# Kernel tuning notes

Measured on AMD Instinct MI355X. Metric: run time of the kernel, lower is better.

## Reference

```python
import jax, jax.numpy as jnp
import numpy as np

N, E, G = 50000, 800000, 500
D, H, L, C, P = 256, 128, 2, 2, 128


def gcn(h, W, b, src, dst, ew, n):
    # PyG GCNConv: x@W, add self-loops (weight 1), sym-normalized aggregation at dst, + bias
    x = h @ W
    deg = jnp.ones((n,), x.dtype).at[dst].add(ew)  # self-loop contributes 1
    dinv = jax.lax.rsqrt(deg)
    norm = dinv[src] * ew * dinv[dst]
    out = jax.ops.segment_sum(x[src] * norm[:, None], dst, num_segments=n)
    out = out + x * (dinv * dinv)[:, None]  # self-loop message
    return out + b


def setup_inputs() -> dict:
    key = jax.random.key(0)
    ks = iter(jax.random.split(key, 64))

    def p(shape, s=0.05):
        return jax.random.normal(next(ks), shape, jnp.float32) * s

    inp = {
        'x': jax.random.normal(next(ks), (N, D), jnp.float32),
        'edge_index': jax.random.randint(next(ks), (2, E), 0, N),
        'edge_weight': jax.random.uniform(next(ks), (E,), jnp.float32),
        'batch': jnp.sort(jax.random.randint(next(ks), (N,), 0, G)),
        'eeg_mask': jax.random.randint(next(ks), (N,), 0, 2).astype(jnp.int32),
        'num_graphs': G,
        'eeg_W': p((D, H)), 'eeg_b': jnp.zeros((H,), jnp.float32),
        'fnirs_W': p((D, H)), 'fnirs_b': jnp.zeros((H,), jnp.float32),
        'edge_W1': p((H + 1, 64)), 'edge_b1': jnp.zeros((64,), jnp.float32),
        'edge_W2': p((64, 1)), 'edge_b2': jnp.zeros((1,), jnp.float32),
        'conv_intra_W': p((L, H, H)), 'conv_intra_b': jnp.zeros((L, H), jnp.float32),
        'conv_cross_W': p((L, H, H)), 'conv_cross_b': jnp.zeros((L, H), jnp.float32),
        'rel_gate': jnp.zeros((L,), jnp.float32),
        'bn_gamma': jnp.ones((L, H), jnp.float32), 'bn_beta': jnp.zeros((L, H), jnp.float32),
        'co_W1': p((3 * H, H)), 'co_b1': jnp.zeros((H,), jnp.float32),
        'co_W2': p((H, 2)), 'co_b2': jnp.zeros((2,), jnp.float32),
        'gate_W1': p((2 * H, H)), 'gate_b1': jnp.zeros((H,), jnp.float32),
        'gate_W2': p((H, 1)), 'gate_b2': jnp.zeros((1,), jnp.float32),
        'cls_W1': p((H, H // 2)), 'cls_b1': jnp.zeros((H // 2,), jnp.float32),
        'cls_W2': p((H // 2, C)), 'cls_b2': jnp.zeros((C,), jnp.float32),
        'pe_W1': p((H, H)), 'pe_b1': jnp.zeros((H,), jnp.float32),
        'pe_W2': p((H, P)), 'pe_b2': jnp.zeros((P,), jnp.float32),
        'pf_W1': p((H, H)), 'pf_b1': jnp.zeros((H,), jnp.float32),
        'pf_W2': p((H, P)), 'pf_b2': jnp.zeros((P,), jnp.float32),
    }
    return inp


def reference(x, edge_index, edge_weight, batch, eeg_mask, num_graphs,
              eeg_W, eeg_b, fnirs_W, fnirs_b,
              edge_W1, edge_b1, edge_W2, edge_b2,
              conv_intra_W, conv_intra_b, conv_cross_W, conv_cross_b,
              rel_gate, bn_gamma, bn_beta,
              co_W1, co_b1, co_W2, co_b2,
              gate_W1, gate_b1, gate_W2, gate_b2,
              cls_W1, cls_b1, cls_W2, cls_b2,
              pe_W1, pe_b1, pe_W2, pe_b2,
              pf_W1, pf_b1, pf_W2, pf_b2):
    n = x.shape[0]
    src, dst = edge_index[0], edge_index[1]
    em = eeg_mask.astype(bool)
    emf = em.astype(x.dtype)
    # modality-aware projection (select per node)
    h = jnp.where(em[:, None], jax.nn.relu(x @ eeg_W + eeg_b), jax.nn.relu(x @ fnirs_W + fnirs_b))
    # edge modulation: MLP on (|h_src - h_dst|, w)
    diff = jnp.abs(h[src] - h[dst])  # [E, H]
    eh = jax.nn.relu(jnp.concatenate([diff, edge_weight[:, None]], axis=1) @ edge_W1 + edge_b1)
    g = jax.nn.sigmoid((eh @ edge_W2 + edge_b2)[:, 0])
    ew_hat = edge_weight * jnp.clip(g, 0.2, 1.2)
    # intra/cross relation split via weight masking (same math as edge subsetting)
    intra = (em[src] == em[dst]).astype(x.dtype)
    ew_intra = ew_hat * intra
    ew_cross = ew_hat * (1.0 - intra)
    for l in range(conv_intra_W.shape[0]):
        hi = gcn(h, conv_intra_W[l], conv_intra_b[l], src, dst, ew_intra, n)
        hc = gcn(h, conv_cross_W[l], conv_cross_b[l], src, dst, ew_cross, n)
        h = hi + jax.nn.sigmoid(rel_gate[l]) * hc
        mu = h.mean(0)
        var = h.var(0)  # biased, as in torch BN training
        h = bn_gamma[l] * (h - mu) * jax.lax.rsqrt(var + 1e-5) + bn_beta[l]
        h = jax.nn.relu(h)  # dropout: eval mode (identity)

    def pool(w):
        s = jax.ops.segment_sum(h * w[:, None], batch, num_segments=num_graphs)
        c = jax.ops.segment_sum(w, batch, num_segments=num_graphs)
        return s / jnp.maximum(c, 1.0)[:, None]

    h_global = pool(jnp.ones((n,), x.dtype))
    h_e = pool(emf)
    h_f = pool(1.0 - emf)
    co = jnp.concatenate([h_e, h_f, h_e * h_f], axis=-1)
    alpha = jax.nn.sigmoid(jax.nn.relu(co @ co_W1 + co_b1) @ co_W2 + co_b2)
    alpha = alpha / (alpha.sum(-1, keepdims=True) + 1e-6)
    h_cr = alpha[:, :1] * h_e + alpha[:, 1:] * h_f
    gte = jax.nn.sigmoid(jax.nn.relu(jnp.concatenate([h_cr, h_global], -1) @ gate_W1 + gate_b1) @ gate_W2 + gate_b2)
    h_final = gte * h_cr + (1.0 - gte) * h_global
    logits = jax.nn.relu(h_final @ cls_W1 + cls_b1) @ cls_W2 + cls_b2

    def l2n(z):
        return z / jnp.maximum(jnp.linalg.norm(z, axis=-1, keepdims=True), 1e-12)

    z_e = l2n(jax.nn.relu(h_e @ pe_W1 + pe_b1) @ pe_W2 + pe_b2)
    z_f = l2n(jax.nn.relu(h_f @ pf_W1 + pf_b1) @ pf_W2 + pf_b2)
    return logits, z_e, z_f
```

## Files before the change

### kernel.cpp

```cpp
#include <hip/hip_runtime.h>
#include <math.h>

#define H 128
#define D 256

typedef __attribute__((ext_vector_type(8))) short bf16x8;
typedef __attribute__((ext_vector_type(4))) float f32x4;

__device__ __forceinline__ float sigmoidf_(float x){ return 1.0f/(1.0f+__expf(-x)); }

__device__ __forceinline__ unsigned int bfr_(float f){
  unsigned int u = __float_as_uint(f);
  return (u + 0x7fffu + ((u>>16)&1u)) >> 16;
}

__device__ __forceinline__ void split2(float a, float b, unsigned &hi, unsigned &lo){
  unsigned ha = bfr_(a), hb2 = bfr_(b);
  float fa = __uint_as_float(ha<<16), fb = __uint_as_float(hb2<<16);
  unsigned la = bfr_(a - fa), lb = bfr_(b - fb);
  hi = ha | (hb2<<16); lo = la | (lb<<16);
}

__device__ __forceinline__ unsigned pair_dft(unsigned a, unsigned b){
  float a0 = __uint_as_float(a<<16), a1 = __uint_as_float(a & 0xffff0000u);
  float b0 = __uint_as_float(b<<16), b1 = __uint_as_float(b & 0xffff0000u);
  unsigned d0 = __float_as_uint(fabsf(a0-b0));
  unsigned d1 = __float_as_uint(fabsf(a1-b1));
  return __builtin_amdgcn_perm(d1, d0, 0x07060302);
}

__global__ void k_prepall(const float* __restrict__ eegW, const float* __restrict__ fnW,
                          const float* __restrict__ cIW, const float* __restrict__ cCW,
                          const float* __restrict__ eW1,
                          unsigned short* WeF, unsigned short* WfF,
                          unsigned short* WIf0, unsigned short* WCf0,
                          unsigned short* WIf1, unsigned short* WCf1,
                          unsigned short* W1b)
{
  int b = blockIdx.x;
  int t = threadIdx.x;
  if (b < 64){
    const float* W; unsigned short* out; int ksteps; int boff;
    if (b < 16){ W=eegW; out=WeF; ksteps=8; boff=b; }
    else if (b < 32){ W=fnW; out=WfF; ksteps=8; boff=b-16; }
    else if (b < 40){ W=cIW;        out=WIf0; ksteps=4; boff=b-32; }
    else if (b < 48){ W=cCW;        out=WCf0; ksteps=4; boff=b-40; }
    else if (b < 56){ W=cIW+16384;  out=WIf1; ksteps=4; boff=b-48; }
    else            { W=cCW+16384;  out=WCf1; ksteps=4; boff=b-56; }
    int id = boff*256 + t;
    if (id >= ksteps*8*64) return;
    int lane = id & 63;
    int mfrag = (id>>6) & 7;
    int kstep = id >> 9;
    int col = mfrag*16 + (lane&15);
    int k0 = kstep*32 + (lane>>4)*8;
    unsigned short* oh = out + (size_t)(((kstep*8+mfrag)*2+0)*64 + lane)*8;
    unsigned short* ol = out + (size_t)(((kstep*8+mfrag)*2+1)*64 + lane)*8;
    #pragma unroll
    for (int j=0;j<8;j++){
      float w = W[(size_t)(k0+j)*128 + col];
      unsigned h16 = bfr_(w);
      float hf = __uint_as_float(h16<<16);
      oh[j] = (unsigned short)h16;
      ol[j] = (unsigned short)bfr_(w - hf);
    }
  } else {
    for (int it=0; it<4; it++){
      int le = it*256 + t;
      int f = le >> 6, lane = le & 63;
      int kstep = f >> 2, n = f & 3;
      int col = n*16 + (lane & 15);
      int k0 = kstep*32 + ((lane>>4)&3)*8;
      unsigned short* op = W1b + (size_t)le*8;
      #pragma unroll
      for (int j=0;j<8;j++)
        op[j] = (unsigned short)bfr_(eW1[(size_t)(k0+j)*64 + col]);
    }
  }
}

__global__ __launch_bounds__(256) void k_projm(
    const float* __restrict__ x, const int* __restrict__ em,
    const unsigned short* __restrict__ WeF, const float* __restrict__ be,
    const unsigned short* __restrict__ WfF, const float* __restrict__ bf,
    float* __restrict__ h, unsigned int* __restrict__ hb, int N)
{
  int t = threadIdx.x;
  int lane = t & 63;
  int base = (blockIdx.x*4 + (t>>6))*16;
  if (base >= N) return;
  int node = base + (lane & 15);
  int nodeL = min(node, N-1);
  int ko = lane >> 4;

  f32x4 accE[8], accF[8];
  #pragma unroll
  for (int mf=0;mf<8;mf++){ accE[mf]=(f32x4){0.f,0.f,0.f,0.f}; accF[mf]=(f32x4){0.f,0.f,0.f,0.f}; }

  const bf16x8* we = reinterpret_cast<const bf16x8*>(WeF);
  const bf16x8* wf = reinterpret_cast<const bf16x8*>(WfF);
  const float4* xr0 = reinterpret_cast<const float4*>(x + (size_t)nodeL*D + ko*8);

  float4 nv0 = xr0[0], nv1 = xr0[1];
  #pragma unroll
  for (int kstep=0;kstep<8;kstep++){
    float4 v0 = nv0, v1 = nv1;
    if (kstep < 7){
      nv0 = xr0[(kstep+1)*8];
      nv1 = xr0[(kstep+1)*8 + 1];
    }
    uint4 hiu, lou;
    split2(v0.x, v0.y, hiu.x, lou.x);
    split2(v0.z, v0.w, hiu.y, lou.y);
    split2(v1.x, v1.y, hiu.z, lou.z);
    split2(v1.z, v1.w, hiu.w, lou.w);
    bf16x8 Bhi = *reinterpret_cast<bf16x8*>(&hiu);
    bf16x8 Blo = *reinterpret_cast<bf16x8*>(&lou);
    #pragma unroll
    for (int mf=0;mf<8;mf++){
      int fb = (kstep*8+mf)*2;
      bf16x8 aEh = we[(size_t)fb*64 + lane];
      bf16x8 aEl = we[(size_t)(fb+1)*64 + lane];
      accE[mf] = __builtin_amdgcn_mfma_f32_16x16x32_bf16(aEh, Bhi, accE[mf], 0,0,0);
      accE[mf] = __builtin_amdgcn_mfma_f32_16x16x32_bf16(aEh, Blo, accE[mf], 0,0,0);
      accE[mf] = __builtin_amdgcn_mfma_f32_16x16x32_bf16(aEl, Bhi, accE[mf], 0,0,0);
      bf16x8 aFh = wf[(size_t)fb*64 + lane];
      bf16x8 aFl = wf[(size_t)(fb+1)*64 + lane];
      accF[mf] = __builtin_amdgcn_mfma_f32_16x16x32_bf16(aFh, Bhi, accF[mf], 0,0,0);
      accF[mf] = __builtin_amdgcn_mfma_f32_16x16x32_bf16(aFh, Blo, accF[mf], 0,0,0);
      accF[mf] = __builtin_amdgcn_mfma_f32_16x16x32_bf16(aFl, Bhi, accF[mf], 0,0,0);
    }
  }
  if (node >= N) return;
  bool e = em[node] != 0;
  #pragma unroll
  for (int mf=0;mf<8;mf++){
    float sv[4];
    #pragma unroll
    for (int r=0;r<4;r++){
      int ch = mf*16 + ko*4 + r;
      float vE = accE[mf][r] + be[ch];
      float vF = accF[mf][r] + bf[ch];
      sv[r] = fmaxf(e ? vE : vF, 0.f);
    }
    float2* hp = reinterpret_cast<float2*>(h + (size_t)node*H + mf*16 + ko*4);
    hp[0] = make_float2(sv[0], sv[1]);
    hp[1] = make_float2(sv[2], sv[3]);
    unsigned int* hbp = hb + (size_t)node*64 + mf*8 + ko*2;
    hbp[0] = bfr_(sv[0]) | (bfr_(sv[1])<<16);
    hbp[1] = bfr_(sv[2]) | (bfr_(sv[3])<<16);
  }
}

__global__ __launch_bounds__(256) void k_gemm2m(
    const float* __restrict__ A,
    const unsigned short* __restrict__ WIf, const unsigned short* __restrict__ WCf,
    const float* __restrict__ bna, const float* __restrict__ bnb2,
    unsigned int* __restrict__ tIb, unsigned int* __restrict__ tCb, int N)
{
  int t = threadIdx.x;
  int lane = t & 63;
  int base = (blockIdx.x*4 + (t>>6))*16;
  if (base >= N) return;
  int node = base + (lane & 15);
  int nodeL = min(node, N-1);
  int ko = lane >> 4;

  f32x4 accI[8], accC[8];
  #pragma unroll
  for (int mf=0;mf<8;mf++){ accI[mf]=(f32x4){0.f,0.f,0.f,0.f}; accC[mf]=(f32x4){0.f,0.f,0.f,0.f}; }

  const bf16x8* wi = reinterpret_cast<const bf16x8*>(WIf);
  const bf16x8* wc = reinterpret_cast<const bf16x8*>(WCf);
  bool doBN = (bna != nullptr);

  #pragma unroll
  for (int kstep=0;kstep<4;kstep++){
    const float4* ar = reinterpret_cast<const float4*>(A + (size_t)nodeL*H + kstep*32 + ko*8);
    float4 v0 = ar[0], v1 = ar[1];
    if (doBN){
      int ch = kstep*32 + ko*8;
      const float4* a4 = reinterpret_cast<const float4*>(bna + ch);
      const float4* b4 = reinterpret_cast<const float4*>(bnb2 + ch);
      float4 a0 = a4[0], a1 = a4[1], bb0 = b4[0], bb1 = b4[1];
      v0.x = fmaxf(fmaf(a0.x, v0.x, bb0.x), 0.f);
      v0.y = fmaxf(fmaf(a0.y, v0.y, bb0.y), 0.f);
      v0.z = fmaxf(fmaf(a0.z, v0.z, bb0.z), 0.f);
      v0.w = fmaxf(fmaf(a0.w, v0.w, bb0.w), 0.f);
      v1.x = fmaxf(fmaf(a1.x, v1.x, bb1.x), 0.f);
      v1.y = fmaxf(fmaf(a1.y, v1.y, bb1.y), 0.f);
      v1.z = fmaxf(fmaf(a1.z, v1.z, bb1.z), 0.f);
      v1.w = fmaxf(fmaf(a1.w, v1.w, bb1.w), 0.f);
    }
    uint4 hiu, lou;
    split2(v0.x, v0.y, hiu.x, lou.x);
    split2(v0.z, v0.w, hiu.y, lou.y);
    split2(v1.x, v1.y, hiu.z, lou.z);
    split2(v1.z, v1.w, hiu.w, lou.w);
    bf16x8 Bhi = *reinterpret_cast<bf16x8*>(&hiu);
    bf16x8 Blo = *reinterpret_cast<bf16x8*>(&lou);
    #pragma unroll
    for (int mf=0;mf<8;mf++){
      int fb = (kstep*8+mf)*2;
      bf16x8 aIh = wi[(size_t)fb*64 + lane];
      bf16x8 aIl = wi[(size_t)(fb+1)*64 + lane];
      accI[mf] = __builtin_amdgcn_mfma_f32_16x16x32_bf16(aIh, Bhi, accI[mf], 0,0,0);
      accI[mf] = __builtin_amdgcn_mfma_f32_16x16x32_bf16(aIh, Blo, accI[mf], 0,0,0);
      accI[mf] = __builtin_amdgcn_mfma_f32_16x16x32_bf16(aIl, Bhi, accI[mf], 0,0,0);
      bf16x8 aCh = wc[(size_t)fb*64 + lane];
      bf16x8 aCl = wc[(size_t)(fb+1)*64 + lane];
      accC[mf] = __builtin_amdgcn_mfma_f32_16x16x32_bf16(aCh, Bhi, accC[mf], 0,0,0);
      accC[mf] = __builtin_amdgcn_mfma_f32_16x16x32_bf16(aCh, Blo, accC[mf], 0,0,0);
      accC[mf] = __builtin_amdgcn_mfma_f32_16x16x32_bf16(aCl, Bhi, accC[mf], 0,0,0);
    }
  }
  if (node >= N) return;
  #pragma unroll
  for (int mf=0;mf<8;mf++){
    unsigned int* ti = tIb + (size_t)node*64 + mf*8 + ko*2;
    unsigned int* tc = tCb + (size_t)node*64 + mf*8 + ko*2;
    ti[0] = bfr_(accI[mf][0]) | (bfr_(accI[mf][1])<<16);
    ti[1] = bfr_(accI[mf][2]) | (bfr_(accI[mf][3])<<16);
    tc[0] = bfr_(accC[mf][0]) | (bfr_(accC[mf][1])<<16);
    tc[1] = bfr_(accC[mf][2]) | (bfr_(accC[mf][3])<<16);
  }
}

__global__ void k_hist(const int* __restrict__ ei, int* __restrict__ cnt, int E){
  int e = blockIdx.x*blockDim.x + threadIdx.x;
  if (e < E) atomicAdd(cnt + ei[E+e], 1);
}

__global__ __launch_bounds__(1024) void k_scanA(const int* __restrict__ cnt,
                                                int* __restrict__ start,
                                                int* __restrict__ bsum, int N){
  __shared__ int wsum[16];
  int t = threadIdx.x;
  int lane = t & 63, wid = t >> 6;
  int i = blockIdx.x*1024 + t;
  int v = (i < N) ? cnt[i] : 0;
  int s = v;
  #pragma unroll
  for (int d=1; d<64; d<<=1){
    int u = __shfl_up(s, d, 64);
    if (lane >= d) s += u;
  }
  if (lane == 63) wsum[wid] = s;
  __syncthreads();
  if (wid == 0){
    int w = (lane < 16) ? wsum[lane] : 0;
    #pragma unroll
    for (int d=1; d<16; d<<=1){
      int u = __shfl_up(w, d, 64);
      if (lane >= d) w += u;
    }
    if (lane < 16) wsum[lane] = w;
  }
  __syncthreads();
  int incl = s + ((wid > 0) ? wsum[wid-1] : 0);
  if (i < N) start[i] = incl - v;
  if (t == 1023) bsum[blockIdx.x] = incl;
}

__global__ __launch_bounds__(1024) void k_scanC(int* __restrict__ start,
                                                const int* __restrict__ bsum,
                                                int N, int nb){
  int b = blockIdx.x, t = threadIdx.x;
  int o = 0;
  for (int j=0;j<b;j++) o += bsum[j];
  int i = b*1024 + t;
  if (i < N) start[i] += o;
  if (b == nb-1 && t == 0) start[N] = o + bsum[b];
}

__global__ void k_fill2(const int* __restrict__ ei, const int* __restrict__ em,
                        const float* __restrict__ ew,
                        const int* __restrict__ start, int* __restrict__ wcnt,
                        int* __restrict__ csr_sc, int* __restrict__ csr_d,
                        float* __restrict__ csr_w, int E){
  int e = blockIdx.x*blockDim.x + threadIdx.x;
  if (e >= E) return;
  int s = ei[e], d = ei[E+e];
  int chan = (em[s] == em[d]) ? 0 : 1;
  int pos = start[d] + atomicAdd(wcnt + d, 1);
  csr_sc[pos] = (s<<1) | chan;
  csr_d[pos] = d;
  csr_w[pos] = ew[e];
}

__global__ __launch_bounds__(256) void k_edgem(
    const unsigned int* __restrict__ hb,
    const int* __restrict__ csr_sc, const int* __restrict__ csr_d,
    const float* __restrict__ csr_w, const unsigned short* __restrict__ W1b,
    const float* __restrict__ W1, const float* __restrict__ b1,
    const float* __restrict__ W2, const float* __restrict__ b2,
    float* __restrict__ csr_cf,
    float* __restrict__ degI, float* __restrict__ degC, int E)
{
  __shared__ uint4 wlds[1024];
  int t = threadIdx.x;
  {
    const uint4* src = reinterpret_cast<const uint4*>(W1b);
    #pragma unroll
    for (int i=0;i<4;i++) wlds[i*256 + t] = src[i*256 + t];
  }
  __syncthreads();

  int lane = t & 63;
  int base0 = (blockIdx.x*4 + (t>>6)) * 32;
  if (base0 >= E) return;

  int colbase = lane & 15;
  int ko = lane >> 4;
  float w1l[4], b1v[4], w2v[4];
  #pragma unroll
  for (int n=0;n<4;n++){
    int col = n*16 + colbase;
    w1l[n] = W1[(size_t)128*64 + col];
    b1v[n] = b1[col];
    w2v[n] = W2[col];
  }
  float bb2 = b2[0];

  uint4 us[2][4], ud[2][4];
  #pragma unroll
  for (int eg=0; eg<2; eg++){
    int e = min(base0 + eg*16 + colbase, E-1);
    int s = csr_sc[e] >> 1;
    int d = csr_d[e];
    const uint4* hsp = reinterpret_cast<const uint4*>(hb + (size_t)s*64);
    const uint4* hdp = reinterpret_cast<const uint4*>(hb + (size_t)d*64);
    #pragma unroll
    for (int kstep=0;kstep<4;kstep++){
      us[eg][kstep] = hsp[kstep*4 + ko];
      ud[eg][kstep] = hdp[kstep*4 + ko];
    }
  }

  const bf16x8* wl = reinterpret_cast<const bf16x8*>(wlds);
  #pragma unroll
  for (int eg=0; eg<2; eg++){
    int base = base0 + eg*16;
    if (base >= E) break;

    f32x4 acc[4];
    #pragma unroll
    for (int n=0;n<4;n++) acc[n] = (f32x4){0.f,0.f,0.f,0.f};

    #pragma unroll
    for (int kstep=0;kstep<4;kstep++){
      uint4 pa;
      pa.x = pair_dft(us[eg][kstep].x, ud[eg][kstep].x);
      pa.y = pair_dft(us[eg][kstep].y, ud[eg][kstep].y);
      pa.z = pair_dft(us[eg][kstep].z, ud[eg][kstep].z);
      pa.w = pair_dft(us[eg][kstep].w, ud[eg][kstep].w);
      bf16x8 a = *reinterpret_cast<bf16x8*>(&pa);
      #pragma unroll
      for (int n=0;n<4;n++)
        acc[n] = __builtin_amdgcn_mfma_f32_16x16x32_bf16(a, wl[(kstep*4+n)*64 + lane], acc[n], 0,0,0);
    }

    float wgtr[4];
    #pragma unroll
    for (int r=0;r<4;r++)
      wgtr[r] = csr_w[min(base + ko*4 + r, E-1)];

    float part[4] = {0.f,0.f,0.f,0.f};
    #pragma unroll
    for (int n=0;n<4;n++){
      #pragma unroll
      for (int r=0;r<4;r++){
        float v = fmaxf(acc[n][r] + fmaf(wgtr[r], w1l[n], b1v[n]), 0.f);
        part[r] = fmaf(v, w2v[n], part[r]);
      }
    }
    #pragma unroll
    for (int m=1;m<16;m<<=1){
      #pragma unroll
      for (int r=0;r<4;r++) part[r] += __shfl_xor(part[r], m, 64);
    }

    if (colbase == 0){
      #pragma unroll
      for (int r=0;r<4;r++){
        int ee = base + ko*4 + r;
        if (ee < E){
          float g = sigmoidf_(part[r] + bb2);
          g = fminf(fmaxf(g, 0.2f), 1.2f);
          float ehat = wgtr[r] * g;
          csr_cf[ee] = ehat;
          int sc2 = csr_sc[ee];
          atomicAdd(((sc2&1) ? degC : degI) + csr_d[ee], ehat);
        }
      }
    }
  }
}

__global__ void k_dinv(const float* __restrict__ degI, const float* __restrict__ degC,
                       float* dinvI, float* dinvC, int N){
  int i = blockIdx.x*blockDim.x + threadIdx.x;
  if (i < N){
    dinvI[i] = rsqrtf(1.f + degI[i]);
    dinvC[i] = rsqrtf(1.f + degC[i]);
  }
}

__global__ void k_scale(const int* __restrict__ csr_sc, const int* __restrict__ csr_d,
                        const float* __restrict__ dinvI, const float* __restrict__ dinvC,
                        float* __restrict__ csr_cf, int E){
  int k = blockIdx.x*blockDim.x + threadIdx.x;
  if (k >= E) return;
  int sc = csr_sc[k];
  int s = sc>>1;
  int d = csr_d[k];
  const float* dv = (sc&1) ? dinvC : dinvI;
  csr_cf[k] *= dv[s]*dv[d];
}

__global__ void k_bnab(const float* __restrict__ bnsum, const float* __restrict__ bnsq,
                       const float* __restrict__ gamma, const float* __restrict__ beta,
                       float invN, float* __restrict__ bna, float* __restrict__ bnb2){
  int j = threadIdx.x;
  float mu = bnsum[j]*invN;
  float var = bnsq[j]*invN - mu*mu;
  float r = rsqrtf(var + 1e-5f);
  float a = gamma[j]*r;
  bna[j] = a;
  bnb2[j] = beta[j] - a*mu;
}

__global__ __launch_bounds__(256) void k_aggrb(
    const unsigned int* __restrict__ tIb, const unsigned int* __restrict__ tCb,
    const int* __restrict__ start, const int* __restrict__ csr_sc,
    const float* __restrict__ csr_cf,
    const float* __restrict__ dinvI, const float* __restrict__ dinvC,
    const float* __restrict__ bI, const float* __restrict__ bC,
    const float* __restrict__ relg, int l,
    float* __restrict__ h, int N)
{
  int lane = threadIdx.x & 63;
  int d = blockIdx.x*4 + (threadIdx.x>>6);
  if (d >= N) return;
  float sig = sigmoidf_(relg[l]);
  int k0 = start[d], k1 = start[d+1];
  float ax=0.f, ay=0.f;
  int k = k0;
  for (; k+8 <= k1; k += 8){
    unsigned vv[8]; float cc[8];
    #pragma unroll
    for (int u=0;u<8;u++){
      int sc = csr_sc[k+u];
      float cf = csr_cf[k+u];
      vv[u] = ((sc&1) ? tCb : tIb)[(size_t)(sc>>1)*64 + lane];
      cc[u] = (sc&1) ? sig*cf : cf;
    }
    #pragma unroll
    for (int u=0;u<8;u++){
      ax = fmaf(cc[u], __uint_as_float(vv[u]<<16), ax);
      ay = fmaf(cc[u], __uint_as_float(vv[u] & 0xffff0000u), ay);
    }
  }
  for (; k < k1; ++k){
    int sc = csr_sc[k];
    float cf = csr_cf[k];
    unsigned v = ((sc&1) ? tCb : tIb)[(size_t)(sc>>1)*64 + lane];
    float ce = (sc&1) ? sig*cf : cf;
    ax = fmaf(ce, __uint_as_float(v<<16), ax);
    ay = fmaf(ce, __uint_as_float(v & 0xffff0000u), ay);
  }
  float diI = dinvI[d], diC = dinvC[d];
  float rI = diI*diI, rC = diC*diC;
  unsigned vi = tIb[(size_t)d*64 + lane];
  unsigned vc = tCb[(size_t)d*64 + lane];
  int off = lane*2;
  float ox = fmaf(__uint_as_float(vi<<16), rI, bI[off])
           + sig*fmaf(__uint_as_float(vc<<16), rC, bC[off]) + ax;
  float oy = fmaf(__uint_as_float(vi & 0xffff0000u), rI, bI[off+1])
           + sig*fmaf(__uint_as_float(vc & 0xffff0000u), rC, bC[off+1]) + ay;
  *reinterpret_cast<float2*>(h + (size_t)d*H + off) = make_float2(ox, oy);
}

__global__ __launch_bounds__(128) void k_stats(const float* __restrict__ h,
    float* __restrict__ bnsum, float* __restrict__ bnsq, int N, int nper)
{
  int j = threadIdx.x;
  int n0 = blockIdx.x*nper, n1 = min(n0+nper, N);
  if (n0 >= N) return;
  float sl=0.f, sq=0.f;
  for (int n=n0;n<n1;n++){
    float v = h[(size_t)n*H+j];
    sl += v; sq = fmaf(v,v,sq);
  }
  atomicAdd(bnsum+j, sl); atomicAdd(bnsq+j, sq);
}

__global__ __launch_bounds__(128) void k_poolbn(
    const float* __restrict__ h, const int* __restrict__ batch, const int* __restrict__ em,
    const float* __restrict__ bnsum, const float* __restrict__ bnsq,
    const float* __restrict__ gamma, const float* __restrict__ beta, float invN,
    float* __restrict__ sumE, float* __restrict__ sumF,
    float* __restrict__ cntE, float* __restrict__ cntF, int N, int nper)
{
  int j = threadIdx.x;
  int n0 = blockIdx.x*nper, n1 = min(n0+nper, N);
  if (n0 >= N) return;
  float mu = bnsum[j]*invN;
  float var = bnsq[j]*invN - mu*mu;
  float rr = rsqrtf(var + 1e-5f);
  float ga = gamma[j], be = beta[j];
  float aE=0.f, aF=0.f, ce=0.f, cfc=0.f;
  int cg = batch[n0];
  for (int n=n0;n<n1;n++){
    int g = batch[n];
    if (g != cg){
      atomicAdd(sumE+(size_t)cg*H+j, aE);
      atomicAdd(sumF+(size_t)cg*H+j, aF);
      if (j==0){ atomicAdd(cntE+cg, ce); atomicAdd(cntF+cg, cfc); }
      aE=aF=ce=cfc=0.f; cg=g;
    }
    float v = fmaxf(fmaf(ga, (h[(size_t)n*H+j]-mu)*rr, be), 0.f);
    bool eb = em[n] != 0;
    if (eb) aE += v; else aF += v;
    if (j==0){ if (eb) ce += 1.f; else cfc += 1.f; }
  }
  atomicAdd(sumE+(size_t)cg*H+j, aE);
  atomicAdd(sumF+(size_t)cg*H+j, aF);
  if (j==0){ atomicAdd(cntE+cg, ce); atomicAdd(cntF+cg, cfc); }
}

__device__ __forceinline__ float blockReduceSum(float v, float* red){
  int t = threadIdx.x;
  red[t] = v; __syncthreads();
  #pragma unroll
  for (int s=64;s>0;s>>=1){ if (t<s) red[t]+=red[t+s]; __syncthreads(); }
  float r = red[0]; __syncthreads();
  return r;
}

__global__ __launch_bounds__(128) void k_head(
    const float* __restrict__ sumE, const float* __restrict__ sumF,
    const float* __restrict__ cntE, const float* __restrict__ cntF,
    const float* __restrict__ coW1, const float* __restrict__ cob1,
    const float* __restrict__ coW2, const float* __restrict__ cob2,
    const float* __restrict__ gW1, const float* __restrict__ gb1,
    const float* __restrict__ gW2, const float* __restrict__ gb2,
    const float* __restrict__ cW1, const float* __restrict__ cb1,
    const float* __restrict__ cW2, const float* __restrict__ cb2,
    const float* __restrict__ peW1, const float* __restrict__ peb1,
    const float* __restrict__ peW2, const float* __restrict__ peb2,
    const float* __restrict__ pfW1, const float* __restrict__ pfb1,
    const float* __restrict__ pfW2, const float* __restrict__ pfb2,
    float* __restrict__ out, int G)
{
  int g = blockIdx.x, j = threadIdx.x;
  __shared__ float sh[384];
  __shared__ float red[128];
  __shared__ float hfin[128], buf[128];
  float cE = cntE[g], cF = cntF[g];
  float se = sumE[(size_t)g*H+j], sf = sumF[(size_t)g*H+j];
  float he = se/fmaxf(cE,1.f), hf = sf/fmaxf(cF,1.f);
  float hg = (se+sf)/fmaxf(cE+cF,1.f);
  sh[j]=he; sh[128+j]=hf; sh[256+j]=he*hf;
  __syncthreads();
  float a = cob1[j];
  for (int k=0;k<384;k++) a = fmaf(sh[k], coW1[k*H+j], a);
  a = fmaxf(a, 0.f);
  float r0 = blockReduceSum(a*coW2[2*j],   red);
  float r1 = blockReduceSum(a*coW2[2*j+1], red);
  float al0 = sigmoidf_(r0 + cob2[0]);
  float al1 = sigmoidf_(r1 + cob2[1]);
  float asum = al0+al1+1e-6f; al0/=asum; al1/=asum;
  float hc = al0*he + al1*hf;
  __syncthreads();
  sh[j]=hc; sh[128+j]=hg;
  __syncthreads();
  float gg = gb1[j];
  for (int k=0;k<256;k++) gg = fmaf(sh[k], gW1[k*H+j], gg);
  gg = fmaxf(gg, 0.f);
  float gt = sigmoidf_(blockReduceSum(gg*gW2[j], red) + gb2[0]);
  float hfj = gt*hc + (1.f-gt)*hg;
  hfin[j] = hfj;
  __syncthreads();
  float c1v = 0.f;
  if (j < 64){
    float c1 = cb1[j];
    for (int k=0;k<128;k++) c1 = fmaf(hfin[k], cW1[k*64+j], c1);
    c1v = fmaxf(c1, 0.f);
  }
  float l0 = blockReduceSum(j<64 ? c1v*cW2[2*j]   : 0.f, red);
  float l1 = blockReduceSum(j<64 ? c1v*cW2[2*j+1] : 0.f, red);
  if (j==0){ out[(size_t)g*2] = l0 + cb2[0]; out[(size_t)g*2+1] = l1 + cb2[1]; }
  buf[j] = he; __syncthreads();
  float q = peb1[j];
  for (int k=0;k<128;k++) q = fmaf(buf[k], peW1[k*H+j], q);
  q = fmaxf(q, 0.f);
  __syncthreads(); sh[j] = q; __syncthreads();
  float z = peb2[j];
  for (int k=0;k<128;k++) z = fmaf(sh[k], peW2[k*H+j], z);
  float nr = sqrtf(blockReduceSum(z*z, red));
  out[(size_t)G*2 + (size_t)g*H + j] = z / fmaxf(nr, 1e-12f);
  __syncthreads(); buf[j] = hf; __syncthreads();
  float q2 = pfb1[j];
  for (int k=0;k<128;k++) q2 = fmaf(buf[k], pfW1[k*H+j], q2);
  q2 = fmaxf(q2, 0.f);
  __syncthreads(); sh[j] = q2; __syncthreads();
  float z2 = pfb2[j];
  for (int k=0;k<128;k++) z2 = fmaf(sh[k], pfW2[k*H+j], z2);
  float nr2 = sqrtf(blockReduceSum(z2*z2, red));
  out[(size_t)G*2 + (size_t)G*H + (size_t)g*H + j] = z2 / fmaxf(nr2, 1e-12f);
}

extern "C" void kernel_launch(void* const* d_in, const int* in_sizes, int n_in,
                              void* d_out, int out_size, void* d_ws, size_t ws_size,
                              hipStream_t stream)
{
  const float* x    = (const float*)d_in[0];
  const int*   ei   = (const int*)d_in[1];
  const float* ew   = (const float*)d_in[2];
  const int*   batch= (const int*)d_in[3];
  const int*   em   = (const int*)d_in[4];
  const float* eegW = (const float*)d_in[6];  const float* eegB = (const float*)d_in[7];
  const float* fnW  = (const float*)d_in[8];  const float* fnB  = (const float*)d_in[9];
  const float* eW1  = (const float*)d_in[10]; const float* eb1  = (const float*)d_in[11];
  const float* eW2  = (const float*)d_in[12]; const float* eb2  = (const float*)d_in[13];
  const float* cIW  = (const float*)d_in[14]; const float* cIb  = (const float*)d_in[15];
  const float* cCW  = (const float*)d_in[16]; const float* cCb  = (const float*)d_in[17];
  const float* relg = (const float*)d_in[18];
  const float* bng  = (const float*)d_in[19]; const float* bnb  = (const float*)d_in[20];
  const float* coW1 = (const float*)d_in[21]; const float* cob1 = (const float*)d_in[22];
  const float* coW2 = (const float*)d_in[23]; const float* cob2 = (const float*)d_in[24];
  const float* gW1  = (const float*)d_in[25]; const float* gb1  = (const float*)d_in[26];
  const float* gW2  = (const float*)d_in[27]; const float* gb2  = (const float*)d_in[28];
  const float* cW1  = (const float*)d_in[29]; const float* cb1  = (const float*)d_in[30];
  const float* cW2  = (const float*)d_in[31]; const float* cb2  = (const float*)d_in[32];
  const float* peW1 = (const float*)d_in[33]; const float* peb1 = (const float*)d_in[34];
  const float* peW2 = (const float*)d_in[35]; const float* peb2 = (const float*)d_in[36];
  const float* pfW1 = (const float*)d_in[37]; const float* pfb1 = (const float*)d_in[38];
  const float* pfW2 = (const float*)d_in[39]; const float* pfb2 = (const float*)d_in[40];
  float* out = (float*)d_out;

  int N = in_sizes[0] / D;
  int E = in_sizes[2];
  int G = out_size / (2 + 2*H);
  int NH = N*H;

  float* p = (float*)d_ws;
  float* h    = p; p += (size_t)NH;
  float* tI   = p; p += (size_t)NH;
  float* tC   = p; p += (size_t)NH;
  float* csr_cf = p; p += E;
  float* csr_w  = p; p += E;
  int* csr_sc = (int*)p; p += E;
  int* csr_d  = (int*)p; p += E;
  int* start  = (int*)p; p += (N+1);
  int* cnt    = (int*)p; p += N;
  int* wcnt   = (int*)p; p += N;
  float* degI = p; p += N;
  float* degC = p; p += N;
  float* dinvI= p; p += N;
  float* dinvC= p; p += N;
  float* bnsum= p; p += H;
  float* bnsq = p; p += H;
  float* bna  = p; p += H;
  float* bnb2 = p; p += H;
  float* sumE = p; p += (size_t)G*H;
  float* sumF = p; p += (size_t)G*H;
  float* cntE = p; p += G;
  float* cntF = p; p += G;
  int* bsum   = (int*)p; p += 64;
  unsigned short* W1b = (unsigned short*)p; p += 4096;
  unsigned short* WeF = (unsigned short*)p; p += 32768;
  unsigned short* WfF = (unsigned short*)p; p += 32768;
  unsigned short* WIf0= (unsigned short*)p; p += 16384;
  unsigned short* WCf0= (unsigned short*)p; p += 16384;
  unsigned short* WIf1= (unsigned short*)p; p += 16384;
  unsigned short* WCf1= (unsigned short*)p; p += 16384;

  unsigned int* hb  = (unsigned int*)tI;
  unsigned int* tIb = (unsigned int*)tI;
  unsigned int* tCb = (unsigned int*)tC;

  int mmBlocks = ((N+15)/16 + 3)/4;
  int edgeBlocks = (E + 127)/128;
  int statBlocks = 1024;
  int nper_stat = (N + statBlocks - 1)/statBlocks;
  int poolBlocks = (N + 31)/32;
  int scanBlocks = (N + 1023)/1024;

  hipMemsetAsync(cnt, 0, (size_t)4*N*sizeof(int), stream);
  k_hist<<<(E+255)/256,256,0,stream>>>(ei, cnt, E);
  k_scanA<<<scanBlocks,1024,0,stream>>>(cnt, start, bsum, N);
  k_scanC<<<scanBlocks,1024,0,stream>>>(start, bsum, N, scanBlocks);
  k_fill2<<<(E+255)/256,256,0,stream>>>(ei, em, ew, start, wcnt,
                                        csr_sc, csr_d, csr_w, E);
  k_prepall<<<65,256,0,stream>>>(eegW, fnW, cIW, cCW, eW1,
                                 WeF, WfF, WIf0, WCf0, WIf1, WCf1, W1b);

  k_projm<<<mmBlocks,256,0,stream>>>(x, em, WeF, eegB, WfF, fnB, h, hb, N);
  k_edgem<<<edgeBlocks,256,0,stream>>>(hb, csr_sc, csr_d, csr_w, W1b,
                                       eW1, eb1, eW2, eb2, csr_cf, degI, degC, E);
  k_dinv<<<(N+255)/256,256,0,stream>>>(degI,degC,dinvI,dinvC,N);
  k_scale<<<(E+255)/256,256,0,stream>>>(csr_sc, csr_d, dinvI, dinvC, csr_cf, E);

  k_gemm2m<<<mmBlocks,256,0,stream>>>(h, WIf0, WCf0, nullptr, nullptr, tIb, tCb, N);
  k_aggrb<<<(N+3)/4,256,0,stream>>>(tIb, tCb, start, csr_sc, csr_cf,
                                    dinvI, dinvC, cIb, cCb, relg, 0, h, N);
  hipMemsetAsync(bnsum, 0, 2*H*sizeof(float), stream);
  k_stats<<<statBlocks,128,0,stream>>>(h, bnsum, bnsq, N, nper_stat);
  k_bnab<<<1,128,0,stream>>>(bnsum, bnsq, bng, bnb, 1.0f/(float)N, bna, bnb2);

  k_gemm2m<<<mmBlocks,256,0,stream>>>(h, WIf1, WCf1, bna, bnb2, tIb, tCb, N);
  k_aggrb<<<(N+3)/4,256,0,stream>>>(tIb, tCb, start, csr_sc, csr_cf,
                                    dinvI, dinvC, cIb+(size_t)H, cCb+(size_t)H,
                                    relg, 1, h, N);
  hipMemsetAsync(bnsum, 0, 2*H*sizeof(float), stream);
  k_stats<<<statBlocks,128,0,stream>>>(h, bnsum, bnsq, N, nper_stat);

  hipMemsetAsync(sumE, 0, ((size_t)2*G*H + 2*G)*sizeof(float), stream);
  k_poolbn<<<poolBlocks,128,0,stream>>>(h, batch, em, bnsum, bnsq,
                                        bng+(size_t)H, bnb+(size_t)H, 1.0f/(float)N,
                                        sumE, sumF, cntE, cntF, N, 32);
  k_head<<<G,128,0,stream>>>(sumE,sumF,cntE,cntF,
                             coW1,cob1,coW2,cob2, gW1,gb1,gW2,gb2,
                             cW1,cb1,cW2,cb2, peW1,peb1,peW2,peb2,
                             pfW1,pfb1,pfW2,pfb2, out, G);
}
```

Before: 597.5 us.

## Partition nodes by modality so projection computes only the selected weight GEMM

Adds a scan over the EEG mask and a partition kernel that builds a node list with EEG nodes first and fNIRS nodes after, each segment padded to multiples of 16. The projection kernel then picks one weight matrix per 16-node tile and runs a single GEMM instead of computing both EEG and fNIRS projections for every node and discarding one. This halves the MFMA work and weight loads in projection. In exchange it adds three small kernel launches, turns the x reads into gathers through the node list, and drops the software prefetch of the next x chunk.

```diff
diff --git a/kernel.cpp b/kernel.cpp
--- a/kernel.cpp
+++ b/kernel.cpp
@@ -79,36 +79,53 @@
   }
 }
 
+__global__ void k_part(const int* __restrict__ em, const int* __restrict__ escan,
+                       int* __restrict__ nodelist, int N){
+  int i = blockIdx.x*blockDim.x + threadIdx.x;
+  int NE = escan[N];
+  int NEpad = (NE+15)&~15;
+  if (i < N){
+    int pos = em[i] ? escan[i] : NEpad + (i - escan[i]);
+    nodelist[pos] = i;
+  }
+  if (i < 16){
+    if (NE + i < NEpad) nodelist[NE + i] = 0;
+    int TOT = NEpad + (N - NE);
+    int TOTpad = (TOT+15)&~15;
+    if (TOT + i < TOTpad) nodelist[TOT + i] = 0;
+  }
+}
+
 __global__ __launch_bounds__(256) void k_projm(
-    const float* __restrict__ x, const int* __restrict__ em,
+    const float* __restrict__ x, const int* __restrict__ nodelist,
+    const int* __restrict__ escan, int N,
     const unsigned short* __restrict__ WeF, const float* __restrict__ be,
     const unsigned short* __restrict__ WfF, const float* __restrict__ bf,
-    float* __restrict__ h, unsigned int* __restrict__ hb, int N)
+    float* __restrict__ h, unsigned int* __restrict__ hb)
 {
   int t = threadIdx.x;
   int lane = t & 63;
   int base = (blockIdx.x*4 + (t>>6))*16;
-  if (base >= N) return;
-  int node = base + (lane & 15);
-  int nodeL = min(node, N-1);
+  int NE = escan[N];
+  int NEpad = (NE+15)&~15;
+  int TOT = NEpad + (N - NE);
+  if (base >= TOT) return;
+  bool isE = (base < NEpad);
+  int slot = base + (lane & 15);
+  bool valid = isE ? (slot < NE) : (slot < TOT);
+  int node = nodelist[slot];
   int ko = lane >> 4;
 
-  f32x4 accE[8], accF[8];
-  #pragma unroll
-  for (int mf=0;mf<8;mf++){ accE[mf]=(f32x4){0.f,0.f,0.f,0.f}; accF[mf]=(f32x4){0.f,0.f,0.f,0.f}; }
-
-  const bf16x8* we = reinterpret_cast<const bf16x8*>(WeF);
-  const bf16x8* wf = reinterpret_cast<const bf16x8*>(WfF);
-  const float4* xr0 = reinterpret_cast<const float4*>(x + (size_t)nodeL*D + ko*8);
-
-  float4 nv0 = xr0[0], nv1 = xr0[1];
-  #pragma unroll
+  f32x4 acc[8];
+  #pragma unroll
+  for (int mf=0;mf<8;mf++) acc[mf]=(f32x4){0.f,0.f,0.f,0.f};
+
+  const bf16x8* wsel = reinterpret_cast<const bf16x8*>(isE ? WeF : WfF);
+  const float* bsel = isE ? be : bf;
+  const float4* xr0 = reinterpret_cast<const float4*>(x + (size_t)node*D + ko*8);
+
   for (int kstep=0;kstep<8;kstep++){
-    float4 v0 = nv0, v1 = nv1;
-    if (kstep < 7){
-      nv0 = xr0[(kstep+1)*8];
-      nv1 = xr0[(kstep+1)*8 + 1];
-    }
+    float4 v0 = xr0[kstep*8], v1 = xr0[kstep*8 + 1];
     uint4 hiu, lou;
     split2(v0.x, v0.y, hiu.x, lou.x);
     split2(v0.z, v0.w, hiu.y, lou.y);
@@ -119,29 +136,21 @@
     #pragma unroll
     for (int mf=0;mf<8;mf++){
       int fb = (kstep*8+mf)*2;
-      bf16x8 aEh = we[(size_t)fb*64 + lane];
-      bf16x8 aEl = we[(size_t)(fb+1)*64 + lane];
-      accE[mf] = __builtin_amdgcn_mfma_f32_16x16x32_bf16(aEh, Bhi, accE[mf], 0,0,0);
-      accE[mf] = __builtin_amdgcn_mfma_f32_16x16x32_bf16(aEh, Blo, accE[mf], 0,0,0);
-      accE[mf] = __builtin_amdgcn_mfma_f32_16x16x32_bf16(aEl, Bhi, accE[mf], 0,0,0);
-      bf16x8 aFh = wf[(size_t)fb*64 + lane];
-      bf16x8 aFl = wf[(size_t)(fb+1)*64 + lane];
-      accF[mf] = __builtin_amdgcn_mfma_f32_16x16x32_bf16(aFh, Bhi, accF[mf], 0,0,0);
-      accF[mf] = __builtin_amdgcn_mfma_f32_16x16x32_bf16(aFh, Blo, accF[mf], 0,0,0);
-      accF[mf] = __builtin_amdgcn_mfma_f32_16x16x32_bf16(aFl, Bhi, accF[mf], 0,0,0);
-    }
-  }
-  if (node >= N) return;
-  bool e = em[node] != 0;
+      bf16x8 ah = wsel[(size_t)fb*64 + lane];
+      bf16x8 al = wsel[(size_t)(fb+1)*64 + lane];
+      acc[mf] = __builtin_amdgcn_mfma_f32_16x16x32_bf16(ah, Bhi, acc[mf], 0,0,0);
+      acc[mf] = __builtin_amdgcn_mfma_f32_16x16x32_bf16(ah, Blo, acc[mf], 0,0,0);
+      acc[mf] = __builtin_amdgcn_mfma_f32_16x16x32_bf16(al, Bhi, acc[mf], 0,0,0);
+    }
+  }
+  if (!valid) return;
   #pragma unroll
   for (int mf=0;mf<8;mf++){
     float sv[4];
     #pragma unroll
     for (int r=0;r<4;r++){
       int ch = mf*16 + ko*4 + r;
-      float vE = accE[mf][r] + be[ch];
-      float vF = accF[mf][r] + bf[ch];
-      sv[r] = fmaxf(e ? vE : vF, 0.f);
+      sv[r] = fmaxf(acc[mf][r] + bsel[ch], 0.f);
     }
     float2* hp = reinterpret_cast<float2*>(h + (size_t)node*H + mf*16 + ko*4);
     hp[0] = make_float2(sv[0], sv[1]);
@@ -669,6 +678,9 @@
   float* cntE = p; p += G;
   float* cntF = p; p += G;
   int* bsum   = (int*)p; p += 64;
+  int* bsum2  = (int*)p; p += 64;
+  int* escan  = (int*)p; p += (N+1);
+  int* nodelist = (int*)p; p += (N+32);
   unsigned short* W1b = (unsigned short*)p; p += 4096;
   unsigned short* WeF = (unsigned short*)p; p += 32768;
   unsigned short* WfF = (unsigned short*)p; p += 32768;
@@ -682,6 +694,7 @@
   unsigned int* tCb = (unsigned int*)tC;
 
   int mmBlocks = ((N+15)/16 + 3)/4;
+  int projBlocks = (((N+32)/16) + 3)/4;
   int edgeBlocks = (E + 127)/128;
   int statBlocks = 1024;
   int nper_stat = (N + statBlocks - 1)/statBlocks;
@@ -692,12 +705,16 @@
   k_hist<<<(E+255)/256,256,0,stream>>>(ei, cnt, E);
   k_scanA<<<scanBlocks,1024,0,stream>>>(cnt, start, bsum, N);
   k_scanC<<<scanBlocks,1024,0,stream>>>(start, bsum, N, scanBlocks);
+  k_scanA<<<scanBlocks,1024,0,stream>>>(em, escan, bsum2, N);
+  k_scanC<<<scanBlocks,1024,0,stream>>>(escan, bsum2, N, scanBlocks);
+  k_part<<<(N+255)/256,256,0,stream>>>(em, escan, nodelist, N);
   k_fill2<<<(E+255)/256,256,0,stream>>>(ei, em, ew, start, wcnt,
                                         csr_sc, csr_d, csr_w, E);
   k_prepall<<<65,256,0,stream>>>(eegW, fnW, cIW, cCW, eW1,
                                  WeF, WfF, WIf0, WCf0, WIf1, WCf1, W1b);
 
-  k_projm<<<mmBlocks,256,0,stream>>>(x, em, WeF, eegB, WfF, fnB, h, hb, N);
+  k_projm<<<projBlocks,256,0,stream>>>(x, nodelist, escan, N,
+                                       WeF, eegB, WfF, fnB, h, hb);
   k_edgem<<<edgeBlocks,256,0,stream>>>(hb, csr_sc, csr_d, csr_w, W1b,
                                        eW1, eb1, eW2, eb2, csr_cf, degI, degC, E);
   k_dinv<<<(N+255)/256,256,0,stream>>>(degI,degC,dinvI,dinvC,N);
```

Result: faster. 560.8 us (-6.1%).
